# Optimization experiments

Hardware: AMD Instinct MI355X
Metric: run time of the kernel (lower is better)

The kernel has to match this reference:

```python
import jax, jax.numpy as jnp
import numpy as np

BN_EPS = 1e-5
K2 = 9  # 3x3 kernel


def _conv3x3(x, w, b):
    # x: [B,C,H,W], w: [O,C,3,3] -> [B,O,H,W], stride 1, pad 1
    out = jax.lax.conv_general_dilated(
        x, w, window_strides=(1, 1), padding=((1, 1), (1, 1)),
        dimension_numbers=("NCHW", "OIHW", "NCHW"))
    return out + b[None, :, None, None]


def setup_inputs() -> dict:
    key = jax.random.key(0)
    ks = jax.random.split(key, 8)
    B, C, H, W = 8, 256, 64, 64
    O = 256
    x = jax.random.normal(ks[0], (B, C, H, W), dtype=jnp.float32)
    # offset/mask conv: small init so sampled offsets stay near the base grid
    w_off = jax.random.normal(ks[1], (3 * K2, C, 3, 3), dtype=jnp.float32) * 0.01
    b_off = jnp.zeros((3 * K2,), dtype=jnp.float32)
    weight = jax.random.normal(ks[2], (O, C, 3, 3), dtype=jnp.float32) * 0.02
    bias = jnp.zeros((O,), dtype=jnp.float32)
    gamma = jnp.ones((O,), dtype=jnp.float32)
    beta = jnp.zeros((O,), dtype=jnp.float32)
    run_mean = jax.random.normal(ks[3], (O,), dtype=jnp.float32) * 0.1
    run_var = jax.random.uniform(ks[4], (O,), dtype=jnp.float32) + 0.5
    return {"x": x, "w_off": w_off, "b_off": b_off, "weight": weight,
            "bias": bias, "gamma": gamma, "beta": beta,
            "run_mean": run_mean, "run_var": run_var}


def _deform_sample(img, py, px):
    # img: [C,H,W]; py, px: [K2,H,W] sampling coordinates.
    # Bilinear sample with zero padding outside (DCNv2 semantics:
    # out-of-bounds corners contribute zero).
    C, H, W = img.shape
    y0 = jnp.floor(py)
    x0 = jnp.floor(px)
    wy1 = py - y0  # frac weights for the 'high' corner
    wx1 = px - x0

    def gather(yi, xi):
        valid = (yi >= 0) & (yi < H) & (xi >= 0) & (xi < W)
        yc = jnp.clip(yi, 0, H - 1).astype(jnp.int32)
        xc = jnp.clip(xi, 0, W - 1).astype(jnp.int32)
        return img[:, yc, xc] * valid.astype(img.dtype)[None]  # [C,K2,H,W]

    v00 = gather(y0, x0)
    v01 = gather(y0, x0 + 1)
    v10 = gather(y0 + 1, x0)
    v11 = gather(y0 + 1, x0 + 1)
    return (v00 * ((1 - wy1) * (1 - wx1))[None]
            + v01 * ((1 - wy1) * wx1)[None]
            + v10 * (wy1 * (1 - wx1))[None]
            + v11 * (wy1 * wx1)[None])  # [C,K2,H,W]


def reference(x, w_off, b_off, weight, bias, gamma, beta, run_mean, run_var):
    B, C, H, W = x.shape
    O = weight.shape[0]
    # 1) offset / mask branch (standard 3x3 conv)
    om = _conv3x3(x, w_off, b_off)  # [B, 27, H, W]
    off_y = om[:, :K2]
    off_x = om[:, K2:2 * K2]
    mask = jax.nn.sigmoid(om[:, 2 * K2:])  # modulation, [B,9,H,W]
    # 2) base sampling grid for 3x3, stride 1, pad 1, dilation 1
    ky = jnp.repeat(jnp.arange(3), 3).astype(x.dtype)  # [9]
    kx = jnp.tile(jnp.arange(3), 3).astype(x.dtype)    # [9]
    hs = jnp.arange(H, dtype=x.dtype)
    ws = jnp.arange(W, dtype=x.dtype)
    base_y = hs[None, :, None] - 1.0 + ky[:, None, None]  # [9,H,1]
    base_x = ws[None, None, :] - 1.0 + kx[:, None, None]  # [9,1,W]
    py = base_y[None] + off_y  # [B,9,H,W]
    px = base_x[None] + off_x
    # 3) modulated deformable im2col (bilinear gather) per batch
    cols = jax.vmap(_deform_sample)(x, py, px)  # [B,C,9,H,W]
    cols = cols * mask[:, None]                 # apply modulation mask
    # 4) GEMM over (C, K2) + bias
    w3 = weight.reshape(O, C, K2)
    out = jnp.einsum("ock,bckhw->bohw", w3, cols) + bias[None, :, None, None]
    # 5) BatchNorm (eval mode, running stats) + ReLU
    inv = gamma / jnp.sqrt(run_var + BN_EPS)
    out = out * inv[None, :, None, None] + (beta - run_mean * inv)[None, :, None, None]
    return jax.nn.relu(out)
```

## Files before the change

kernel.cpp:

```cpp
#include <hip/hip_runtime.h>
#include <math.h>

#define H 64
#define W 64
#define C 256
#define O 256
#define CK 2304
#define NB 8
#define HWSZ 4096

typedef __attribute__((ext_vector_type(8))) short short8;
typedef __attribute__((ext_vector_type(4))) float floatx4;
typedef __attribute__((ext_vector_type(4))) unsigned uintx4;
typedef __attribute__((ext_vector_type(2))) float f32x2;

#define FSWZ(n) ((((n) & 3) << 1) | (((n) >> 2) & 1))

__device__ __forceinline__ float lo2f(unsigned u) {
  return __builtin_bit_cast(float, u << 16);
}
__device__ __forceinline__ float hi2f(unsigned u) {
  return __builtin_bit_cast(float, u & 0xffff0000u);
}
__device__ __forceinline__ f32x2 up2(unsigned u) {
  return (f32x2){lo2f(u), hi2f(u)};
}
__device__ __forceinline__ unsigned pk2bf(float v0, float v1) {
  unsigned a = __builtin_bit_cast(unsigned, v0);
  unsigned b = __builtin_bit_cast(unsigned, v1);
  return ((a + 0x8000u) >> 16) | ((b + 0x8000u) & 0xffff0000u);
}

__device__ __forceinline__ f32x2 pk_mul(f32x2 a, f32x2 b) {
  f32x2 d;
  asm("v_pk_mul_f32 %0, %1, %2" : "=v"(d) : "v"(a), "v"(b));
  return d;
}
__device__ __forceinline__ f32x2 pk_fma(f32x2 a, f32x2 b, f32x2 c) {
  f32x2 d;
  asm("v_pk_fma_f32 %0, %1, %2, %3" : "=v"(d) : "v"(a), "v"(b), "v"(c));
  return d;
}
__device__ __forceinline__ unsigned cvtpk(f32x2 a) {
  unsigned d;
  asm("v_cvt_pk_bf16_f32 %0, %1, %2" : "=v"(d) : "v"(a[0]), "v"(a[1]));
  return d;
}

__global__ __launch_bounds__(512) void prep_all2(
    const float* __restrict__ x, const float* __restrict__ weight,
    const float* __restrict__ w_off, const float* __restrict__ bias,
    const float* __restrict__ gamma, const float* __restrict__ beta,
    const float* __restrict__ run_mean, const float* __restrict__ run_var,
    unsigned short* __restrict__ xt, unsigned short* __restrict__ wb,
    unsigned short* __restrict__ wob, float* __restrict__ invsh) {
  __shared__ unsigned tile[16384];
  int bid = blockIdx.x;
  int tid = threadIdx.x;

  if (bid < 256) {
    int b = bid >> 5;
    int yg = bid & 31;
    int y0 = yg * 2;
#pragma unroll
    for (int j = 0; j < 4; ++j) {
      int e = tid + 512 * j;
      int xx4 = e & 15;
      int cp = e >> 4;
      const float* p0 = x + ((size_t)b * C + 2 * cp) * HWSZ + y0 * W + xx4 * 4;
      floatx4 f00 = *reinterpret_cast<const floatx4*>(p0);
      floatx4 f01 = *reinterpret_cast<const floatx4*>(p0 + W);
      floatx4 f10 = *reinterpret_cast<const floatx4*>(p0 + HWSZ);
      floatx4 f11 = *reinterpret_cast<const floatx4*>(p0 + HWSZ + W);
      int sw = cp & 31;
#pragma unroll
      for (int k = 0; k < 4; ++k) {
        int px = xx4 * 4 + k;
        tile[cp * 64 + (px ^ sw)] = pk2bf(f00[k], f10[k]);
        tile[8192 + cp * 64 + (px ^ sw)] = pk2bf(f01[k], f11[k]);
      }
    }
    __syncthreads();
    unsigned short* xo = xt + ((size_t)(b * 64 + y0) << 14);
#pragma unroll
    for (int j = 0; j < 8; ++j) {
      int e = tid + 512 * j;
      int cq = e & 31;
      int xx = (e >> 5) & 63;
      int r = e >> 11;
      unsigned u[4];
#pragma unroll
      for (int kk = 0; kk < 4; ++kk) {
        int cpv = cq * 4 + kk;
        u[kk] = tile[r * 8192 + cpv * 64 + (xx ^ (cpv & 31))];
      }
      uint4 v = {u[0], u[1], u[2], u[3]};
      *reinterpret_cast<uint4*>(xo + (r << 14) + (xx << 8) + (cq << 3)) = v;
    }
  } else if (bid < 400) {
    int idx = (bid - 256) * 512 + tid;
    int d0 = idx * 8;
    int lane = idx & 63;
    int mt = (idx >> 6) & 15;
    int ks = idx >> 10;
    int o = mt * 16 + (lane & 15);
    int kn0 = ks * 32 + (lane >> 4) * 8;
    int tap = kn0 >> 8;
    int c0 = kn0 & 255;
    const float* wsrc = weight + o * CK + c0 * 9 + tap;
    unsigned pk[4];
#pragma unroll
    for (int p = 0; p < 4; ++p)
      pk[p] = pk2bf(wsrc[(2 * p) * 9], wsrc[(2 * p + 1) * 9]);
    uint4 v = {pk[0], pk[1], pk[2], pk[3]};
    *reinterpret_cast<uint4*>(wb + d0) = v;
  } else if (bid < 418) {
    int idx = (bid - 400) * 512 + tid;
    int d0 = idx * 8;
    int lane = idx & 63;
    int mt = (idx >> 6) & 1;
    int ks = idx >> 7;
    int o = mt * 16 + (lane & 15);
    int kn0 = ks * 32 + (lane >> 4) * 8;
    int tap = kn0 >> 8;
    int c0 = kn0 & 255;
    uint4 v;
    if (o < 27) {
      const float* wsrc = w_off + o * CK + c0 * 9 + tap;
      unsigned pk[4];
#pragma unroll
      for (int p = 0; p < 4; ++p)
        pk[p] = pk2bf(wsrc[(2 * p) * 9], wsrc[(2 * p + 1) * 9]);
      v = (uint4){pk[0], pk[1], pk[2], pk[3]};
    } else {
      v = (uint4){0, 0, 0, 0};
    }
    *reinterpret_cast<uint4*>(wob + d0) = v;
  } else {
    if (tid < 256) {
      int o = tid;
      float inv = gamma[o] * rsqrtf(run_var[o] + 1e-5f);
      invsh[o] = inv;
      invsh[O + o] = beta[o] + (bias[o] - run_mean[o]) * inv;
    }
  }
}

__global__ __launch_bounds__(512, 2) void deform_mfma_kernel(
    const unsigned short* __restrict__ xt, const unsigned short* __restrict__ wob,
    const float* __restrict__ b_off, const unsigned short* __restrict__ wb,
    const float* __restrict__ invsh, float* __restrict__ out) {
  __shared__ short cols[64 * 256];
  __shared__ float sm_om[27 * 64];
  __shared__ int sbase[576];
  __shared__ float s00[576], s01[576], s10[576], s11[576];

  int tid = threadIdx.x;
  int lane = tid & 63;
  int wvid = tid >> 6;
  int q = lane >> 4;
  int lm = lane & 15;
  int b = blockIdx.x;
  int h = blockIdx.y;
  const unsigned short* xtb = xt + ((size_t)b << 20);

  if (wvid < 4) {
    int mt = wvid & 1;
    int nh = wvid >> 1;
    floatx4 a0[2];
    a0[0] = (floatx4){0.f, 0.f, 0.f, 0.f};
    a0[1] = (floatx4){0.f, 0.f, 0.f, 0.f};
    int pxu[2];
    pxu[0] = (nh * 2 + 0) * 16 + lm;
    pxu[1] = (nh * 2 + 1) * 16 + lm;
    for (int tap = 0; tap < 9; ++tap) {
      int yy = h - 1 + tap / 3;
      bool vy = (yy >= 0) && (yy < H);
      const unsigned short* bp[2];
      bool vv[2];
#pragma unroll
      for (int u = 0; u < 2; ++u) {
        int xx = pxu[u] - 1 + tap % 3;
        vv[u] = vy && (xx >= 0) && (xx < W);
        bp[u] = xtb + ((((yy & 63) << 6) + (xx & 63)) << 8) + q * 8;
      }
#pragma unroll
      for (int s = 0; s < 8; ++s) {
        int ks = tap * 8 + s;
        short8 afrag = *reinterpret_cast<const short8*>(
            wob + (((ks * 2 + mt) * 64 + lane) << 3));
#pragma unroll
        for (int u = 0; u < 2; ++u) {
          short8 bfrag;
          if (vv[u])
            bfrag = *reinterpret_cast<const short8*>(bp[u] + s * 32);
          else
            bfrag = (short8){0, 0, 0, 0, 0, 0, 0, 0};
          a0[u] = __builtin_amdgcn_mfma_f32_16x16x32_bf16(afrag, bfrag, a0[u], 0, 0, 0);
        }
      }
    }
#pragma unroll
    for (int u = 0; u < 2; ++u)
#pragma unroll
      for (int r = 0; r < 4; ++r) {
        int o = mt * 16 + q * 4 + r;
        if (o < 27) sm_om[o * 64 + pxu[u]] = a0[u][r] + b_off[o];
      }
  }
  __syncthreads();

  for (int e = tid; e < 576; e += 512) {
    int n = e & 63;
    int k = e >> 6;
    float oy = sm_om[k * 64 + n];
    float ox = sm_om[(9 + k) * 64 + n];
    float mv = sm_om[(18 + k) * 64 + n];
    float m = 1.0f / (1.0f + __expf(-mv));
    float py = (float)(h - 1 + k / 3) + oy;
    float px = (float)(n - 1 + k % 3) + ox;
    float yf = floorf(py), xf = floorf(px);
    int y0 = (int)yf, x0 = (int)xf;
    float fy = py - yf, fx = px - xf;
    float r0, r1; int yl;
    if (y0 >= 0 && y0 <= H - 2)      { yl = y0;    r0 = 1.f - fy; r1 = fy;       }
    else if (y0 == -1)               { yl = 0;     r0 = fy;       r1 = 0.f;      }
    else if (y0 == H - 1)            { yl = H - 2; r0 = 0.f;      r1 = 1.f - fy; }
    else                             { yl = 0;     r0 = 0.f;      r1 = 0.f;      }
    float c0, c1; int xl;
    if (x0 >= 0 && x0 <= W - 2)      { xl = x0;    c0 = 1.f - fx; c1 = fx;       }
    else if (x0 == -1)               { xl = 0;     c0 = fx;       c1 = 0.f;      }
    else if (x0 == W - 1)            { xl = W - 2; c0 = 0.f;      c1 = 1.f - fx; }
    else                             { xl = 0;     c0 = 0.f;      c1 = 0.f;      }
    r0 *= m; r1 *= m;
    sbase[e] = ((yl << 6) + xl) << 8;
    s00[e] = r0 * c0; s01[e] = r0 * c1;
    s10[e] = r1 * c0; s11[e] = r1 * c1;
  }
  __syncthreads();

  floatx4 acc[2][4];
#pragma unroll
  for (int a = 0; a < 2; ++a)
#pragma unroll
    for (int u = 0; u < 4; ++u) acc[a][u] = (floatx4){0.f, 0.f, 0.f, 0.f};

  int sn = tid >> 3;
  int scb = tid & 7;

  for (int tap = 0; tap < 9; ++tap) {
    if (tap) __syncthreads();
    {
      int ei = tap * 64 + sn;
      int base = sbase[ei];
      float w00 = s00[ei], w01 = s01[ei], w10 = s10[ei], w11 = s11[ei];
      f32x2 W00 = (f32x2){w00, w00};
      f32x2 W01 = (f32x2){w01, w01};
      f32x2 W10 = (f32x2){w10, w10};
      f32x2 W11 = (f32x2){w11, w11};
      const unsigned short* p = xtb + base;
#pragma unroll
      for (int i = 0; i < 4; ++i) {
        int cbw = (i << 3) | scb;
        int co = cbw << 3;
        uintx4 u00 = *reinterpret_cast<const uintx4*>(p + co);
        uintx4 u01 = *reinterpret_cast<const uintx4*>(p + 256 + co);
        uintx4 u10 = *reinterpret_cast<const uintx4*>(p + 16384 + co);
        uintx4 u11 = *reinterpret_cast<const uintx4*>(p + 16640 + co);
        uintx4 res;
#pragma unroll
        for (int jd = 0; jd < 4; ++jd) {
          f32x2 a = pk_mul(up2(u00[jd]), W00);
          a = pk_fma(up2(u01[jd]), W01, a);
          a = pk_fma(up2(u10[jd]), W10, a);
          a = pk_fma(up2(u11[jd]), W11, a);
          res[jd] = cvtpk(a);
        }
        int pos = (cbw ^ FSWZ(sn)) & 31;
        *reinterpret_cast<uintx4*>(&cols[(sn << 8) + (pos << 3)]) = res;
      }
    }
    __syncthreads();

    __builtin_amdgcn_s_setprio(1);
#pragma unroll
    for (int s = 0; s < 8; ++s) {
      int ks = tap * 8 + s;
      short8 afrag[2];
#pragma unroll
      for (int a = 0; a < 2; ++a)
        afrag[a] = *reinterpret_cast<const short8*>(
            wb + (((ks * 16 + wvid * 2 + a) * 64 + lane) << 3));
      short8 bfrag[4];
#pragma unroll
      for (int u = 0; u < 4; ++u) {
        int nn = u * 16 + lm;
        int pos = ((s * 4 + q) ^ FSWZ(nn)) & 31;
        bfrag[u] = *reinterpret_cast<const short8*>(&cols[(nn << 8) + (pos << 3)]);
      }
#pragma unroll
      for (int a = 0; a < 2; ++a)
#pragma unroll
        for (int u = 0; u < 4; ++u)
          acc[a][u] = __builtin_amdgcn_mfma_f32_16x16x32_bf16(
              afrag[a], bfrag[u], acc[a][u], 0, 0, 0);
    }
    __builtin_amdgcn_s_setprio(0);
  }

#pragma unroll
  for (int a = 0; a < 2; ++a) {
#pragma unroll
    for (int u = 0; u < 4; ++u) {
      int nn = u * 16 + lm;
#pragma unroll
      for (int r = 0; r < 4; ++r) {
        int o = (wvid * 2 + a) * 16 + q * 4 + r;
        float v = fmaf(acc[a][u][r], invsh[o], invsh[O + o]);
        out[((size_t)(b * O + o)) * HWSZ + h * W + nn] = fmaxf(v, 0.0f);
      }
    }
  }
}

extern "C" void kernel_launch(void* const* d_in, const int* in_sizes, int n_in,
                              void* d_out, int out_size, void* d_ws, size_t ws_size,
                              hipStream_t stream) {
  const float* x        = (const float*)d_in[0];
  const float* w_off    = (const float*)d_in[1];
  const float* b_off    = (const float*)d_in[2];
  const float* weight   = (const float*)d_in[3];
  const float* bias     = (const float*)d_in[4];
  const float* gamma    = (const float*)d_in[5];
  const float* beta     = (const float*)d_in[6];
  const float* run_mean = (const float*)d_in[7];
  const float* run_var  = (const float*)d_in[8];
  float* out = (float*)d_out;

  char* ws = (char*)d_ws;
  unsigned short* xt = (unsigned short*)ws;
  unsigned short* wbf = (unsigned short*)(ws + 16777216);
  unsigned short* wob = (unsigned short*)(ws + 17956864);
  float* invsh = (float*)(ws + 18104320);

  prep_all2<<<419, 512, 0, stream>>>(x, weight, w_off, bias, gamma, beta,
                                     run_mean, run_var, xt, wbf, wob, invsh);
  {
    dim3 grid(NB, H);
    deform_mfma_kernel<<<grid, 512, 0, stream>>>(xt, wob, b_off, wbf, invsh, out);
  }
}
```

Before: 187.2 us.

## Double-buffer deformable im2col tile to overlap bilinear gather with MFMA

Splits the cols shared buffer into two halves and software-pipelines the tap loop. The bilinear gather loads for tap+1 are issued before the MFMAs of the current tap, and their results are written into the other buffer afterwards. This removes one barrier per tap and hides global-load latency behind matrix work. The cost is double the LDS for cols (sm_om is aliased into it to compensate) and more live registers, which could hurt occupancy at 2 blocks per CU.

```diff
diff --git a/kernel.cpp b/kernel.cpp
--- a/kernel.cpp
+++ b/kernel.cpp
@@ -146,14 +146,80 @@
   }
 }
 
+__device__ __forceinline__ void issue_half(
+    const unsigned short* __restrict__ p, int scb, int half,
+    uintx4 (&u00)[2], uintx4 (&u01)[2], uintx4 (&u10)[2], uintx4 (&u11)[2]) {
+#pragma unroll
+  for (int j = 0; j < 2; ++j) {
+    int co = (((half * 2 + j) << 3) | scb) << 3;
+    u00[j] = *reinterpret_cast<const uintx4*>(p + co);
+    u01[j] = *reinterpret_cast<const uintx4*>(p + 256 + co);
+    u10[j] = *reinterpret_cast<const uintx4*>(p + 16384 + co);
+    u11[j] = *reinterpret_cast<const uintx4*>(p + 16640 + co);
+  }
+}
+
+__device__ __forceinline__ void finish_half(
+    short* __restrict__ colbuf, int sn, int scb, int half,
+    f32x2 w00, f32x2 w01, f32x2 w10, f32x2 w11,
+    const uintx4 (&u00)[2], const uintx4 (&u01)[2],
+    const uintx4 (&u10)[2], const uintx4 (&u11)[2]) {
+#pragma unroll
+  for (int j = 0; j < 2; ++j) {
+    int cbw = ((half * 2 + j) << 3) | scb;
+    uintx4 res;
+#pragma unroll
+    for (int jd = 0; jd < 4; ++jd) {
+      f32x2 a = pk_mul(up2(u00[j][jd]), w00);
+      a = pk_fma(up2(u01[j][jd]), w01, a);
+      a = pk_fma(up2(u10[j][jd]), w10, a);
+      a = pk_fma(up2(u11[j][jd]), w11, a);
+      res[jd] = cvtpk(a);
+    }
+    int pos = (cbw ^ FSWZ(sn)) & 31;
+    *reinterpret_cast<uintx4*>(&colbuf[(sn << 8) + (pos << 3)]) = res;
+  }
+}
+
+__device__ __forceinline__ void mfma_half(
+    int tap, int half, const unsigned short* __restrict__ wb,
+    const short* __restrict__ colbuf, int wvid, int lane, int q, int lm,
+    floatx4 (&acc)[2][4]) {
+  __builtin_amdgcn_s_setprio(1);
+#pragma unroll
+  for (int s2 = 0; s2 < 4; ++s2) {
+    int s = half * 4 + s2;
+    int ks = tap * 8 + s;
+    short8 afrag[2];
+#pragma unroll
+    for (int a = 0; a < 2; ++a)
+      afrag[a] = *reinterpret_cast<const short8*>(
+          wb + (((ks * 16 + wvid * 2 + a) * 64 + lane) << 3));
+    short8 bfrag[4];
+#pragma unroll
+    for (int u = 0; u < 4; ++u) {
+      int nn = u * 16 + lm;
+      int pos = ((s * 4 + q) ^ FSWZ(nn)) & 31;
+      bfrag[u] = *reinterpret_cast<const short8*>(&colbuf[(nn << 8) + (pos << 3)]);
+    }
+#pragma unroll
+    for (int a = 0; a < 2; ++a)
+#pragma unroll
+      for (int u = 0; u < 4; ++u)
+        acc[a][u] = __builtin_amdgcn_mfma_f32_16x16x32_bf16(
+            afrag[a], bfrag[u], acc[a][u], 0, 0, 0);
+  }
+  __builtin_amdgcn_s_setprio(0);
+}
+
 __global__ __launch_bounds__(512, 2) void deform_mfma_kernel(
     const unsigned short* __restrict__ xt, const unsigned short* __restrict__ wob,
     const float* __restrict__ b_off, const unsigned short* __restrict__ wb,
     const float* __restrict__ invsh, float* __restrict__ out) {
-  __shared__ short cols[64 * 256];
-  __shared__ float sm_om[27 * 64];
+  __shared__ short cols[2][64 * 256];
   __shared__ int sbase[576];
   __shared__ float s00[576], s01[576], s10[576], s11[576];
+  float* sm_om = reinterpret_cast<float*>(&cols[0][0]);
 
   int tid = threadIdx.x;
   int lane = tid & 63;
@@ -248,64 +314,42 @@
   int sn = tid >> 3;
   int scb = tid & 7;
 
+  {
+    const unsigned short* p = xtb + sbase[sn];
+    f32x2 w00 = (f32x2){s00[sn], s00[sn]};
+    f32x2 w01 = (f32x2){s01[sn], s01[sn]};
+    f32x2 w10 = (f32x2){s10[sn], s10[sn]};
+    f32x2 w11 = (f32x2){s11[sn], s11[sn]};
+    uintx4 u00[2], u01[2], u10[2], u11[2];
+    issue_half(p, scb, 0, u00, u01, u10, u11);
+    finish_half(cols[0], sn, scb, 0, w00, w01, w10, w11, u00, u01, u10, u11);
+    issue_half(p, scb, 1, u00, u01, u10, u11);
+    finish_half(cols[0], sn, scb, 1, w00, w01, w10, w11, u00, u01, u10, u11);
+  }
+  __syncthreads();
+
   for (int tap = 0; tap < 9; ++tap) {
-    if (tap) __syncthreads();
-    {
-      int ei = tap * 64 + sn;
-      int base = sbase[ei];
-      float w00 = s00[ei], w01 = s01[ei], w10 = s10[ei], w11 = s11[ei];
-      f32x2 W00 = (f32x2){w00, w00};
-      f32x2 W01 = (f32x2){w01, w01};
-      f32x2 W10 = (f32x2){w10, w10};
-      f32x2 W11 = (f32x2){w11, w11};
-      const unsigned short* p = xtb + base;
-#pragma unroll
-      for (int i = 0; i < 4; ++i) {
-        int cbw = (i << 3) | scb;
-        int co = cbw << 3;
-        uintx4 u00 = *reinterpret_cast<const uintx4*>(p + co);
-        uintx4 u01 = *reinterpret_cast<const uintx4*>(p + 256 + co);
-        uintx4 u10 = *reinterpret_cast<const uintx4*>(p + 16384 + co);
-        uintx4 u11 = *reinterpret_cast<const uintx4*>(p + 16640 + co);
-        uintx4 res;
-#pragma unroll
-        for (int jd = 0; jd < 4; ++jd) {
-          f32x2 a = pk_mul(up2(u00[jd]), W00);
-          a = pk_fma(up2(u01[jd]), W01, a);
-          a = pk_fma(up2(u10[jd]), W10, a);
-          a = pk_fma(up2(u11[jd]), W11, a);
-          res[jd] = cvtpk(a);
-        }
-        int pos = (cbw ^ FSWZ(sn)) & 31;
-        *reinterpret_cast<uintx4*>(&cols[(sn << 8) + (pos << 3)]) = res;
-      }
+    short* cur = cols[tap & 1];
+    short* nxt = cols[(tap + 1) & 1];
+    if (tap < 8) {
+      int ei = (tap + 1) * 64 + sn;
+      const unsigned short* p = xtb + sbase[ei];
+      uintx4 u00[2], u01[2], u10[2], u11[2];
+      issue_half(p, scb, 0, u00, u01, u10, u11);
+      mfma_half(tap, 0, wb, cur, wvid, lane, q, lm, acc);
+      f32x2 w00 = (f32x2){s00[ei], s00[ei]};
+      f32x2 w01 = (f32x2){s01[ei], s01[ei]};
+      f32x2 w10 = (f32x2){s10[ei], s10[ei]};
+      f32x2 w11 = (f32x2){s11[ei], s11[ei]};
+      finish_half(nxt, sn, scb, 0, w00, w01, w10, w11, u00, u01, u10, u11);
+      issue_half(p, scb, 1, u00, u01, u10, u11);
+      mfma_half(tap, 1, wb, cur, wvid, lane, q, lm, acc);
+      finish_half(nxt, sn, scb, 1, w00, w01, w10, w11, u00, u01, u10, u11);
+    } else {
+      mfma_half(tap, 0, wb, cur, wvid, lane, q, lm, acc);
+      mfma_half(tap, 1, wb, cur, wvid, lane, q, lm, acc);
     }
     __syncthreads();
-
-    __builtin_amdgcn_s_setprio(1);
-#pragma unroll
-    for (int s = 0; s < 8; ++s) {
-      int ks = tap * 8 + s;
-      short8 afrag[2];
-#pragma unroll
-      for (int a = 0; a < 2; ++a)
-        afrag[a] = *reinterpret_cast<const short8*>(
-            wb + (((ks * 16 + wvid * 2 + a) * 64 + lane) << 3));
-      short8 bfrag[4];
-#pragma unroll
-      for (int u = 0; u < 4; ++u) {
-        int nn = u * 16 + lm;
-        int pos = ((s * 4 + q) ^ FSWZ(nn)) & 31;
-        bfrag[u] = *reinterpret_cast<const short8*>(&cols[(nn << 8) + (pos << 3)]);
-      }
-#pragma unroll
-      for (int a = 0; a < 2; ++a)
-#pragma unroll
-        for (int u = 0; u < 4; ++u)
-          acc[a][u] = __builtin_amdgcn_mfma_f32_16x16x32_bf16(
-              afrag[a], bfrag[u], acc[a][u], 0, 0, 0);
-    }
-    __builtin_amdgcn_s_setprio(0);
   }
 
 #pragma unroll
```

After: 231.1 us. +23.4%, slower.
